# Kernel tuning notes

Measured on AMD Instinct MI355X. Metric: run time of the kernel, lower is better.

Reference implementation:

```python
import jax, jax.numpy as jnp
import numpy as np

HIDDEN = 2048
NH = 32
NKV = 8
HD = HIDDEN // NH  # 64
GROUP = NH // NKV  # 4


def setup_inputs() -> dict:
    key = jax.random.key(0)
    ks = jax.random.split(key, 9)
    s = 1.0 / np.sqrt(HIDDEN)
    x = jax.random.normal(ks[0], (2, 2048, HIDDEN), dtype=jnp.float32)
    Wq = jax.random.uniform(ks[1], (HIDDEN, HIDDEN), jnp.float32, -s, s)
    bq = jax.random.uniform(ks[2], (HIDDEN,), jnp.float32, -s, s)
    Wk = jax.random.uniform(ks[3], (HIDDEN, NKV * HD), jnp.float32, -s, s)
    bk = jax.random.uniform(ks[4], (NKV * HD,), jnp.float32, -s, s)
    Wv = jax.random.uniform(ks[5], (HIDDEN, NKV * HD), jnp.float32, -s, s)
    bv = jax.random.uniform(ks[6], (NKV * HD,), jnp.float32, -s, s)
    Wo = jax.random.uniform(ks[7], (HIDDEN, HIDDEN), jnp.float32, -s, s)
    bo = jax.random.uniform(ks[8], (HIDDEN,), jnp.float32, -s, s)
    return {"x": x, "Wq": Wq, "bq": bq, "Wk": Wk, "bk": bk,
            "Wv": Wv, "bv": bv, "Wo": Wo, "bo": bo}


def reference(x, Wq, bq, Wk, bk, Wv, bv, Wo, bo):
    B, S, D = x.shape
    scale = 1.0 / np.sqrt(HD).astype(np.float32)
    q = (x @ Wq + bq).reshape(B, S, NH, HD).transpose(0, 2, 1, 3)   # [B,H,S,hd]
    k = (x @ Wk + bk).reshape(B, S, NKV, HD).transpose(0, 2, 1, 3)  # [B,KV,S,hd]
    v = (x @ Wv + bv).reshape(B, S, NKV, HD).transpose(0, 2, 1, 3)
    # repeat_interleave KV heads: kv head j serves query heads j*GROUP..(j+1)*GROUP-1
    k = jnp.repeat(k, GROUP, axis=1)  # [B,H,S,hd]
    v = jnp.repeat(v, GROUP, axis=1)
    scores = jnp.einsum('bhqd,bhkd->bhqk', q, k) * scale  # [B,H,S,S]
    w = jax.nn.softmax(scores, axis=-1)
    out = jnp.einsum('bhqk,bhkd->bhqd', w, v)              # [B,H,S,hd]
    out = out.transpose(0, 2, 1, 3).reshape(B, S, D)
    return out @ Wo + bo
```

## Files before the change

### kernel.cpp

```cpp
#include <hip/hip_runtime.h>

#define HID 2048
#define SEQ 2048
#define NH_ 32
#define NKV_ 8
#define HD_ 64

typedef __attribute__((ext_vector_type(8))) short s8v;
typedef __attribute__((ext_vector_type(4))) float f4v;
typedef __attribute__((ext_vector_type(4))) unsigned int u4v;
typedef unsigned int u32;
typedef unsigned short u16;

#define QSCALE 0.18033688011112042f

__device__ __forceinline__ u16 f2bf(float f) {
  u32 u = __builtin_bit_cast(u32, f);
  u = u + 0x7FFFu + ((u >> 16) & 1u);
  return (u16)(u >> 16);
}

__device__ __forceinline__ float hw_exp2(float x) {
  float r;
  asm("v_exp_f32 %0, %1" : "=v"(r) : "v"(x));
  return r;
}

__device__ __forceinline__ void gl_lds16(const void* g, void* l) {
  __builtin_amdgcn_global_load_lds((const __attribute__((address_space(1))) u32*)g,
                                   (__attribute__((address_space(3))) u32*)l, 16, 0, 0);
}

__device__ __forceinline__ void transp_body(const float* __restrict__ W,
                                            u16* __restrict__ Wt, int K, int N,
                                            int bx, int by, int tid) {
  __shared__ float t[64][65];
  const int n0 = bx * 64, k0 = by * 64;
  const int tr = tid >> 4, tc = tid & 15;
#pragma unroll
  for (int i = 0; i < 4; ++i) {
    int r = i * 16 + tr;
    const float4 v = *reinterpret_cast<const float4*>(&W[(size_t)(k0 + r) * N + n0 + tc * 4]);
    t[r][tc * 4 + 0] = v.x; t[r][tc * 4 + 1] = v.y;
    t[r][tc * 4 + 2] = v.z; t[r][tc * 4 + 3] = v.w;
  }
  __syncthreads();
#pragma unroll
  for (int i = 0; i < 4; ++i) {
    int r = i * 16 + tr;
    ushort4 o;
    o.x = f2bf(t[tc * 4 + 0][r]); o.y = f2bf(t[tc * 4 + 1][r]);
    o.z = f2bf(t[tc * 4 + 2][r]); o.w = f2bf(t[tc * 4 + 3][r]);
    *reinterpret_cast<ushort4*>(&Wt[(size_t)(n0 + r) * K + k0 + tc * 4]) = o;
  }
}

__global__ __launch_bounds__(256) void prep_k(const float* __restrict__ x,
                                              const float* __restrict__ Wq,
                                              const float* __restrict__ Wk,
                                              const float* __restrict__ Wv,
                                              const float* __restrict__ Wo,
                                              u16* __restrict__ xb,
                                              u16* __restrict__ wqkvt,
                                              u16* __restrict__ wot) {
  const int bid = blockIdx.x, tid = threadIdx.x;
  if (bid < 8192) {
    const int i = (bid * 256 + tid) * 4;
    const float4 v = *reinterpret_cast<const float4*>(x + i);
    ushort4 o;
    o.x = f2bf(v.x); o.y = f2bf(v.y); o.z = f2bf(v.z); o.w = f2bf(v.w);
    *reinterpret_cast<ushort4*>(xb + i) = o;
  } else if (bid < 8192 + 1024) {
    const int b2 = bid - 8192;
    transp_body(Wq, wqkvt, 2048, 2048, b2 & 31, b2 >> 5, tid);
  } else if (bid < 8192 + 1024 + 256) {
    const int b2 = bid - (8192 + 1024);
    transp_body(Wk, wqkvt + (size_t)2048 * 2048, 2048, 512, b2 & 7, b2 >> 3, tid);
  } else if (bid < 8192 + 1024 + 512) {
    const int b2 = bid - (8192 + 1024 + 256);
    transp_body(Wv, wqkvt + (size_t)2560 * 2048, 2048, 512, b2 & 7, b2 >> 3, tid);
  } else {
    const int b2 = bid - (8192 + 1024 + 512);
    transp_body(Wo, wot, 2048, 2048, b2 & 31, b2 >> 5, tid);
  }
}

template <int MODE>
__global__ __launch_bounds__(256) void gemm_k(const u16* __restrict__ A,
                                              const u16* __restrict__ Bt,
                                              const float* __restrict__ b0,
                                              const float* __restrict__ b1,
                                              const float* __restrict__ b2,
                                              void* __restrict__ o0,
                                              void* __restrict__ o1,
                                              void* __restrict__ o2,
                                              int M, int N, int K) {
  __shared__ u16 As[128 * 64];
  __shared__ u16 Bs[128 * 64];
  const int tid = threadIdx.x;
  const int w = tid >> 6, l = tid & 63;
  const int wr = w >> 1, wc = w & 1;
  const int lr = l & 15, lg = l >> 4;
  const int gx = gridDim.x;
  const int nwg = gx * gridDim.y;
  const int lin = blockIdx.x + gx * blockIdx.y;
  const int swz = (lin & 7) * (nwg >> 3) + (lin >> 3);
  const int m0 = (swz / gx) * 128, n0 = (swz % gx) * 128;
  f4v acc[4][4] = {};
  for (int k0 = 0; k0 < K; k0 += 64) {
#pragma unroll
    for (int i = 0; i < 4; ++i) {
      int c = i * 256 + tid;
      int r = c >> 3, p = c & 7;
      gl_lds16(&A[(size_t)(m0 + r) * K + k0 + ((p ^ (r & 7)) * 8)], &As[c * 8]);
      gl_lds16(&Bt[(size_t)(n0 + r) * K + k0 + ((p ^ (r & 7)) * 8)], &Bs[c * 8]);
    }
    __syncthreads();
#pragma unroll
    for (int kc = 0; kc < 2; ++kc) {
      s8v af[4], bf[4];
#pragma unroll
      for (int m = 0; m < 4; ++m)
        af[m] = *reinterpret_cast<const s8v*>(
            &As[(wr * 64 + m * 16 + lr) * 64 + ((((kc << 2) + lg) ^ (lr & 7)) << 3)]);
#pragma unroll
      for (int n = 0; n < 4; ++n)
        bf[n] = *reinterpret_cast<const s8v*>(
            &Bs[(wc * 64 + n * 16 + lr) * 64 + ((((kc << 2) + lg) ^ (lr & 7)) << 3)]);
#pragma unroll
      for (int m = 0; m < 4; ++m)
#pragma unroll
        for (int n = 0; n < 4; ++n)
          acc[m][n] = __builtin_amdgcn_mfma_f32_16x16x32_bf16(af[m], bf[n], acc[m][n], 0, 0, 0);
    }
    __syncthreads();
  }
#pragma unroll
  for (int n = 0; n < 4; ++n) {
    const int col = n0 + wc * 64 + n * 16 + lr;
    float bb, scl = 1.0f;
    if (MODE == 2) {
      bb = b0[col];
    } else {
      if (col < 2048) { bb = b0[col]; scl = QSCALE; }
      else if (col < 2560) { bb = b1[col - 2048]; }
      else { bb = b2[col - 2560]; }
    }
#pragma unroll
    for (int m = 0; m < 4; ++m) {
#pragma unroll
      for (int r = 0; r < 4; ++r) {
        const int row = m0 + wr * 64 + m * 16 + lg * 4 + r;
        const float v = (acc[m][n][r] + bb) * scl;
        if (MODE == 2) {
          ((float*)o0)[(size_t)row * N + col] = v;
        } else {
          const int b = row >> 11, s = row & (SEQ - 1);
          if (col < 2048) {
            const int h = col >> 6, d = col & 63;
            ((u16*)o0)[((((size_t)b * NH_ + h) * SEQ + s) << 6) + d] = f2bf(v);
          } else if (col < 2560) {
            const int kv = (col - 2048) >> 6, d = (col - 2048) & 63;
            ((u16*)o1)[((((size_t)b * NKV_ + kv) * SEQ + s) << 6) + d] = f2bf(v);
          } else {
            const int kv = (col - 2560) >> 6, d = (col - 2560) & 63;
            const int sp = (s & ~31) | (((s >> 2) & 3) << 3) | (((s >> 4) & 1) << 2) | (s & 3);
            ((u16*)o2)[(((size_t)b * NKV_ + kv) * HD_ + d) * SEQ + sp] = f2bf(v);
          }
        }
      }
    }
  }
}

__global__ __launch_bounds__(256) void attn_k(const u16* __restrict__ Q,
                                              const u16* __restrict__ Kg,
                                              const u16* __restrict__ Vt,
                                              u16* __restrict__ Og) {
  __shared__ u16 Ks[128 * 64];
  __shared__ u16 Vs[64 * 128];
  const int tid = threadIdx.x;
  const int w = tid >> 6, l = tid & 63;
  const int lr = l & 15, lg = l >> 4;
  const int lin = blockIdx.x + 16 * (blockIdx.y + 32 * blockIdx.z);
  const int swz = ((lin & 7) << 7) | (lin >> 3);
  const int qt = swz & 15, h = (swz >> 4) & 31, b = swz >> 9;
  const int kvh = h >> 2;
  const u16* Qp = Q + ((((size_t)b * NH_ + h) * SEQ + qt * 128) << 6);
  const u16* Kp = Kg + (((size_t)b * NKV_ + kvh) * SEQ << 6);
  const u16* Vp = Vt + ((size_t)b * NKV_ + kvh) * HD_ * SEQ;

  s8v qf[2][2];
#pragma unroll
  for (int i = 0; i < 2; ++i)
#pragma unroll
    for (int kc = 0; kc < 2; ++kc)
      qf[i][kc] = *reinterpret_cast<const s8v*>(
          &Qp[(w * 32 + i * 16 + lr) * 64 + kc * 32 + lg * 8]);

  const u4v ones_u = {0x3F803F80u, 0x3F803F80u, 0x3F803F80u, 0x3F803F80u};
  const s8v ones8 = __builtin_bit_cast(s8v, ones_u);

  f4v Oacc[2][4] = {};
  f4v den[2] = {};

#define STAGE_K(KT)                                                              \
  {                                                                              \
    _Pragma("unroll") for (int i_ = 0; i_ < 4; ++i_) {                           \
      int c_ = i_ * 256 + tid;                                                   \
      int r_ = c_ >> 3, p_ = c_ & 7;                                             \
      gl_lds16(&Kp[((size_t)((KT) * 128 + r_)) * 64 + ((p_ ^ (r_ & 7)) * 8)],    \
               &Ks[c_ * 8]);                                                     \
    }                                                                            \
  }
#define STAGE_V(KT)                                                              \
  {                                                                              \
    _Pragma("unroll") for (int i_ = 0; i_ < 4; ++i_) {                           \
      int c_ = i_ * 256 + tid;                                                   \
      int r_ = c_ >> 4, p_ = c_ & 15;                                            \
      gl_lds16(&Vp[(size_t)r_ * SEQ + (KT) * 128 + ((p_ ^ (r_ & 15)) * 8)],      \
               &Vs[c_ * 8]);                                                     \
    }                                                                            \
  }

  STAGE_K(0);
  STAGE_V(0);
  __syncthreads();

  const int NT = SEQ / 128;
  for (int kt = 0; kt < NT; ++kt) {
    f4v sc[2][8] = {};
    __builtin_amdgcn_s_setprio(1);
#pragma unroll
    for (int kb = 0; kb < 8; ++kb) {
      const int rk = kb * 16 + lr;
#pragma unroll
      for (int kc = 0; kc < 2; ++kc) {
        s8v kfr = *reinterpret_cast<const s8v*>(
            &Ks[rk * 64 + ((((kc << 2) + lg) ^ (lr & 7)) << 3)]);
#pragma unroll
        for (int i = 0; i < 2; ++i)
          sc[i][kb] = __builtin_amdgcn_mfma_f32_16x16x32_bf16(kfr, qf[i][kc], sc[i][kb], 0, 0, 0);
      }
    }
    __builtin_amdgcn_s_setprio(0);

    __syncthreads();
    if (kt + 1 < NT) STAGE_K(kt + 1);

#pragma unroll
    for (int c = 0; c < 4; ++c) {
      s8v pa[2];
#pragma unroll
      for (int i = 0; i < 2; ++i) {
        const float e0 = hw_exp2(sc[i][2 * c][0]);
        const float e1 = hw_exp2(sc[i][2 * c][1]);
        const float e2 = hw_exp2(sc[i][2 * c][2]);
        const float e3 = hw_exp2(sc[i][2 * c][3]);
        const float e4 = hw_exp2(sc[i][2 * c + 1][0]);
        const float e5 = hw_exp2(sc[i][2 * c + 1][1]);
        const float e6 = hw_exp2(sc[i][2 * c + 1][2]);
        const float e7 = hw_exp2(sc[i][2 * c + 1][3]);
        u32 d0, d1, d2, d3;
        asm("v_cvt_pk_bf16_f32 %0, %1, %2" : "=v"(d0) : "v"(e0), "v"(e1));
        asm("v_cvt_pk_bf16_f32 %0, %1, %2" : "=v"(d1) : "v"(e2), "v"(e3));
        asm("v_cvt_pk_bf16_f32 %0, %1, %2" : "=v"(d2) : "v"(e4), "v"(e5));
        asm("v_cvt_pk_bf16_f32 %0, %1, %2" : "=v"(d3) : "v"(e6), "v"(e7));
        u4v t = {d0, d1, d2, d3};
        pa[i] = __builtin_bit_cast(s8v, t);
      }
      __builtin_amdgcn_s_setprio(1);
#pragma unroll
      for (int i = 0; i < 2; ++i)
        den[i] = __builtin_amdgcn_mfma_f32_16x16x32_bf16(pa[i], ones8, den[i], 0, 0, 0);
#pragma unroll
      for (int df = 0; df < 4; ++df) {
        const int d = df * 16 + lr;
        const int ch = ((c << 2) + lg) ^ lr;
        const s8v vb = *reinterpret_cast<const s8v*>(&Vs[d * 128 + (ch << 3)]);
#pragma unroll
        for (int i = 0; i < 2; ++i)
          Oacc[i][df] = __builtin_amdgcn_mfma_f32_16x16x32_bf16(pa[i], vb, Oacc[i][df], 0, 0, 0);
      }
      __builtin_amdgcn_s_setprio(0);
    }

    __syncthreads();
    if (kt + 1 < NT) STAGE_V(kt + 1);
  }

  const int sbase = qt * 128 + w * 32;
#pragma unroll
  for (int i = 0; i < 2; ++i)
#pragma unroll
    for (int r = 0; r < 4; ++r) {
      const float linv = 1.0f / den[i][r];
      const int srow = sbase + i * 16 + lg * 4 + r;
#pragma unroll
      for (int df = 0; df < 4; ++df)
        Og[((size_t)b * SEQ + srow) * HID + h * 64 + df * 16 + lr] =
            f2bf(Oacc[i][df][r] * linv);
    }
#undef STAGE_K
#undef STAGE_V
}

extern "C" void kernel_launch(void* const* d_in, const int* in_sizes, int n_in,
                              void* d_out, int out_size, void* d_ws, size_t ws_size,
                              hipStream_t stream) {
  (void)in_sizes; (void)n_in; (void)out_size;
  const float* x  = (const float*)d_in[0];
  const float* Wq = (const float*)d_in[1];
  const float* bq = (const float*)d_in[2];
  const float* Wk = (const float*)d_in[3];
  const float* bk = (const float*)d_in[4];
  const float* Wv = (const float*)d_in[5];
  const float* bv = (const float*)d_in[6];
  const float* Wo = (const float*)d_in[7];
  const float* bo = (const float*)d_in[8];
  float* out = (float*)d_out;

  u16* ws    = (u16*)d_ws;
  u16* xb    = ws;
  u16* wqkvt = xb + 8388608;
  u16* wot   = wqkvt + 6291456;
  u16* qb    = wot + 4194304;
  u16* kbuf  = qb + 8388608;
  u16* vtb   = kbuf + 2097152;
  u16* ab    = vtb + 2097152;
  if (ws_size < (size_t)(8388608 + 6291456 + 4194304 + 8388608 + 2097152 +
                         2097152 + 8388608) * 2) return;

  prep_k<<<10752, 256, 0, stream>>>(x, Wq, Wk, Wv, Wo, xb, wqkvt, wot);

  gemm_k<3><<<dim3(24, 32), 256, 0, stream>>>(xb, wqkvt, bq, bk, bv,
                                              qb, kbuf, vtb, 4096, 3072, 2048);

  attn_k<<<dim3(16, 32, 2), 256, 0, stream>>>(qb, kbuf, vtb, ab);

  gemm_k<2><<<dim3(16, 32), 256, 0, stream>>>(ab, wot, bo, nullptr, nullptr,
                                              out, nullptr, nullptr, 4096, 2048, 2048);
}
```

Before: 208.1 us.

## Load K and V fragments directly from global memory, dropping LDS staging

The attention kernel no longer stages K and V tiles into shared memory with async global-to-LDS copies and barriers. Each wave now reads its MFMA operand fragments straight from global memory, relying on L1/L2 caching. This removes the __syncthreads barriers and LDS traffic, but each of the four waves now fetches the same K/V data independently. The loads are no longer prefetched ahead of the compute, so the MFMAs may stall on global latency.

```diff
diff --git a/kernel.cpp b/kernel.cpp
--- a/kernel.cpp
+++ b/kernel.cpp
@@ -177,8 +177,6 @@
                                               const u16* __restrict__ Kg,
                                               const u16* __restrict__ Vt,
                                               u16* __restrict__ Og) {
-  __shared__ u16 Ks[128 * 64];
-  __shared__ u16 Vs[64 * 128];
   const int tid = threadIdx.x;
   const int w = tid >> 6, l = tid & 63;
   const int lr = l & 15, lg = l >> 4;
@@ -204,49 +202,22 @@
   f4v Oacc[2][4] = {};
   f4v den[2] = {};
 
-#define STAGE_K(KT)                                                              \
-  {                                                                              \
-    _Pragma("unroll") for (int i_ = 0; i_ < 4; ++i_) {                           \
-      int c_ = i_ * 256 + tid;                                                   \
-      int r_ = c_ >> 3, p_ = c_ & 7;                                             \
-      gl_lds16(&Kp[((size_t)((KT) * 128 + r_)) * 64 + ((p_ ^ (r_ & 7)) * 8)],    \
-               &Ks[c_ * 8]);                                                     \
-    }                                                                            \
-  }
-#define STAGE_V(KT)                                                              \
-  {                                                                              \
-    _Pragma("unroll") for (int i_ = 0; i_ < 4; ++i_) {                           \
-      int c_ = i_ * 256 + tid;                                                   \
-      int r_ = c_ >> 4, p_ = c_ & 15;                                            \
-      gl_lds16(&Vp[(size_t)r_ * SEQ + (KT) * 128 + ((p_ ^ (r_ & 15)) * 8)],      \
-               &Vs[c_ * 8]);                                                     \
-    }                                                                            \
-  }
-
-  STAGE_K(0);
-  STAGE_V(0);
-  __syncthreads();
-
   const int NT = SEQ / 128;
   for (int kt = 0; kt < NT; ++kt) {
     f4v sc[2][8] = {};
     __builtin_amdgcn_s_setprio(1);
 #pragma unroll
     for (int kb = 0; kb < 8; ++kb) {
-      const int rk = kb * 16 + lr;
-#pragma unroll
-      for (int kc = 0; kc < 2; ++kc) {
-        s8v kfr = *reinterpret_cast<const s8v*>(
-            &Ks[rk * 64 + ((((kc << 2) + lg) ^ (lr & 7)) << 3)]);
-#pragma unroll
-        for (int i = 0; i < 2; ++i)
-          sc[i][kb] = __builtin_amdgcn_mfma_f32_16x16x32_bf16(kfr, qf[i][kc], sc[i][kb], 0, 0, 0);
+      const u16* krow = &Kp[(size_t)(kt * 128 + kb * 16 + lr) * 64];
+      const s8v k0 = *reinterpret_cast<const s8v*>(krow + lg * 8);
+      const s8v k1 = *reinterpret_cast<const s8v*>(krow + 32 + lg * 8);
+#pragma unroll
+      for (int i = 0; i < 2; ++i) {
+        sc[i][kb] = __builtin_amdgcn_mfma_f32_16x16x32_bf16(k0, qf[i][0], sc[i][kb], 0, 0, 0);
+        sc[i][kb] = __builtin_amdgcn_mfma_f32_16x16x32_bf16(k1, qf[i][1], sc[i][kb], 0, 0, 0);
       }
     }
     __builtin_amdgcn_s_setprio(0);
-
-    __syncthreads();
-    if (kt + 1 < NT) STAGE_K(kt + 1);
 
 #pragma unroll
     for (int c = 0; c < 4; ++c) {
@@ -275,18 +246,14 @@
         den[i] = __builtin_amdgcn_mfma_f32_16x16x32_bf16(pa[i], ones8, den[i], 0, 0, 0);
 #pragma unroll
       for (int df = 0; df < 4; ++df) {
-        const int d = df * 16 + lr;
-        const int ch = ((c << 2) + lg) ^ lr;
-        const s8v vb = *reinterpret_cast<const s8v*>(&Vs[d * 128 + (ch << 3)]);
+        const s8v vb = *reinterpret_cast<const s8v*>(
+            &Vp[(size_t)(df * 16 + lr) * SEQ + kt * 128 + c * 32 + lg * 8]);
 #pragma unroll
         for (int i = 0; i < 2; ++i)
           Oacc[i][df] = __builtin_amdgcn_mfma_f32_16x16x32_bf16(pa[i], vb, Oacc[i][df], 0, 0, 0);
       }
       __builtin_amdgcn_s_setprio(0);
     }
-
-    __syncthreads();
-    if (kt + 1 < NT) STAGE_V(kt + 1);
   }
 
   const int sbase = qt * 128 + w * 32;
@@ -301,8 +268,6 @@
         Og[((size_t)b * SEQ + srow) * HID + h * 64 + df * 16 + lr] =
             f2bf(Oacc[i][df][r] * linv);
     }
-#undef STAGE_K
-#undef STAGE_V
 }
 
 extern "C" void kernel_launch(void* const* d_in, const int* in_sizes, int n_in,
```

New measurement: 408.9 us. 1.96x slower.
